# Optimization experiments

Measured on AMD Instinct MI355X. Metric: run time of the kernel, lower is better.

The kernel has to match this reference:

```python
import jax, jax.numpy as jnp
import numpy as np

HEADS = 4
NEG_SLOPE = 0.2  # GATv2Conv default negative_slope and module's LeakyReLU
LN_EPS = 1e-5


def setup_inputs() -> dict:
    key = jax.random.key(0)
    ks = jax.random.split(key, 12)
    N, D, E = 50000, 128, 400000
    H, C = HEADS, D
    s = 0.05
    x = jax.random.normal(ks[0], (N, D), dtype=jnp.float32)
    edge_index = jax.random.randint(ks[1], (2, E), 0, N, dtype=jnp.int64)
    return {
        "x": x,
        "edge_index": edge_index,
        "W_l": jax.random.normal(ks[2], (D, H * C), dtype=jnp.float32) * s,
        "b_l": jnp.zeros((H * C,), jnp.float32),
        "W_r": jax.random.normal(ks[3], (D, H * C), dtype=jnp.float32) * s,
        "b_r": jnp.zeros((H * C,), jnp.float32),
        "att": jax.random.normal(ks[4], (H, C), dtype=jnp.float32) * s,
        "gat_bias": jnp.zeros((C,), jnp.float32),
        "ln_g": jnp.ones((D,), jnp.float32),
        "ln_b": jnp.zeros((D,), jnp.float32),
        "W1": jax.random.normal(ks[5], (D, 2 * D), dtype=jnp.float32) * s,
        "b1": jnp.zeros((2 * D,), jnp.float32),
        "W2": jax.random.normal(ks[6], (2 * D, D), dtype=jnp.float32) * s,
        "b2": jnp.zeros((D,), jnp.float32),
    }


def _gatv2(x, src, dst, W_l, b_l, W_r, b_r, att, gat_bias, N):
    D = x.shape[1]
    H, C = HEADS, D
    xl = (x @ W_l + b_l).reshape(N, H, C)  # source-side projection
    xr = (x @ W_r + b_r).reshape(N, H, C)  # target-side projection
    # per-edge GATv2 score: leaky_relu(x_j + x_i) . att
    e = jax.nn.leaky_relu(xl[src] + xr[dst], NEG_SLOPE)  # [E, H, C]
    alpha = jnp.einsum('ehc,hc->eh', e, att)             # [E, H]
    # segment softmax over destination nodes
    amax = jax.ops.segment_max(alpha, dst, num_segments=N)  # [N, H]
    ex = jnp.exp(alpha - amax[dst])
    denom = jax.ops.segment_sum(ex, dst, num_segments=N)
    w = ex / (denom[dst] + 1e-16)                        # [E, H]
    msg = xl[src] * w[:, :, None]                        # [E, H, C]
    out = jax.ops.segment_sum(msg, dst, num_segments=N)  # [N, H, C]
    return out.mean(axis=1) + gat_bias                   # concat=False -> head mean + bias


def reference(x, edge_index, W_l, b_l, W_r, b_r, att, gat_bias, ln_g, ln_b, W1, b1, W2, b2):
    N = x.shape[0]
    # GATv2Conv default add_self_loops=True
    loops = jnp.arange(N, dtype=edge_index.dtype)
    src = jnp.concatenate([edge_index[0], loops])
    dst = jnp.concatenate([edge_index[1], loops])
    h = x + _gatv2(x, src, dst, W_l, b_l, W_r, b_r, att, gat_bias, N)
    # LayerNorm
    mu = h.mean(-1, keepdims=True)
    var = ((h - mu) ** 2).mean(-1, keepdims=True)
    hn = (h - mu) * jax.lax.rsqrt(var + LN_EPS) * ln_g + ln_b
    # FFN with residual
    ffn = jax.nn.leaky_relu(hn @ W1 + b1, NEG_SLOPE) @ W2 + b2
    return hn + ffn
```

## Files before the change

### kernel.cpp

```cpp
#include <hip/hip_runtime.h>
#include <hip/hip_bf16.h>
#include <stdint.h>

typedef __hip_bfloat16 bf16;
typedef __attribute__((ext_vector_type(8))) short short8;
typedef __attribute__((ext_vector_type(4))) float f32x4;

#define NEG 0.2f
#define LN_EPS 1e-5f

__device__ __host__ __forceinline__ int stdch(int q) {
    return (q & ~63) | (16 * (q & 3)) | ((q & 63) >> 2);
}

__device__ __forceinline__ float bits2f(unsigned b) {
    return __uint_as_float(b << 16);
}
__device__ __forceinline__ float hi2f(unsigned b) {
    return __uint_as_float(b & 0xffff0000u);
}
__device__ __forceinline__ unsigned short f2b_bits(float f) {
    unsigned u = __float_as_uint(f);
    unsigned r = u + 0x7fffu + ((u >> 16) & 1u);
    return (unsigned short)(r >> 16);
}
__device__ __forceinline__ float lrelu(float v) {
    return fmaxf(v, 0.f) + NEG * fminf(v, 0.f);
}
__device__ __forceinline__ void unpack8(uint4 u, float* v) {
    v[0] = bits2f(u.x); v[1] = hi2f(u.x);
    v[2] = bits2f(u.y); v[3] = hi2f(u.y);
    v[4] = bits2f(u.z); v[5] = hi2f(u.z);
    v[6] = bits2f(u.w); v[7] = hi2f(u.w);
}

union S8 { uint4 u; short8 s; unsigned short us[8]; };
__device__ __forceinline__ short8 ld8b(const char* p) {
    S8 c; c.u = *(const uint4*)p; return c.s;
}
__device__ __forceinline__ short8 ld8f(const float* p) {
    float4 a = ((const float4*)p)[0], b = ((const float4*)p)[1];
    S8 c;
    c.us[0] = f2b_bits(a.x); c.us[1] = f2b_bits(a.y);
    c.us[2] = f2b_bits(a.z); c.us[3] = f2b_bits(a.w);
    c.us[4] = f2b_bits(b.x); c.us[5] = f2b_bits(b.y);
    c.us[6] = f2b_bits(b.z); c.us[7] = f2b_bits(b.w);
    return c.s;
}

template <int CTRL>
__device__ __forceinline__ float ror_add16(float x) {
    int xi = __float_as_int(x);
    int r = __builtin_amdgcn_update_dpp(xi, xi, CTRL, 0xf, 0xf, false);
    return x + __int_as_float(r);
}

__global__ void detect_kernel(const unsigned* __restrict__ xw, const int* __restrict__ ei,
                              int* __restrict__ flags, int E) {
    int lane = threadIdx.x;
    int sane = 0;
    for (int k = 0; k < 4; ++k) {
        unsigned short lo = (unsigned short)(xw[k * 64 + lane] & 0xFFFFu);
        int ex = (lo >> 7) & 0xFF;
        if (lo == 0 || (ex > 100 && ex < 155)) sane++;
    }
#pragma unroll
    for (int off = 32; off > 0; off >>= 1) sane += __shfl_xor(sane, off);
    int nchk = E < 64 ? E : 64;
    int bad = (lane < nchk) ? (ei[2 * lane + 1] != 0) : 0;
    unsigned long long bb = __ballot(bad);
    if (lane == 0) {
        flags[0] = (sane > 200) ? 1 : 0;
        flags[1] = (bb == 0ULL) ? 1 : 0;
    }
}

struct PrepArgs {
    const void* Wl; const void* Wr; const void* W1; const void* W2;
    const void* ssrc[8];
    const int* ei;
    unsigned short* Wlt; unsigned short* Wrt; unsigned short* W1t; unsigned short* W2x;
    float* smalls;
    int* deg;
    int N; int E;
};
__device__ __forceinline__ float cvt_one(const void* p, int idx, int isb) {
    return isb ? bits2f(((const unsigned short*)p)[idx]) : ((const float*)p)[idx];
}
__global__ __launch_bounds__(256) void prep_kernel(PrepArgs a, const int* __restrict__ flags) {
    int isb = flags[0];
    int i = blockIdx.x * 256 + threadIdx.x;
    int seg = blockIdx.y;
    if (seg == 0) {
        if (i < 512 * 128) {
            int c = i >> 7, k = i & 127;
            a.Wlt[i] = isb ? ((const unsigned short*)a.Wl)[k * 512 + c]
                           : f2b_bits(((const float*)a.Wl)[k * 512 + c]);
        }
    } else if (seg == 1) {
        if (i < 512 * 128) {
            int c = i >> 7, k = i & 127;
            a.Wrt[i] = isb ? ((const unsigned short*)a.Wr)[k * 512 + c]
                           : f2b_bits(((const float*)a.Wr)[k * 512 + c]);
        }
    } else if (seg == 2) {
        if (i < 256 * 128) {
            int c = i >> 7, q = i & 127;
            int k = stdch(q);
            a.W1t[i] = isb ? ((const unsigned short*)a.W1)[k * 256 + c]
                           : f2b_bits(((const float*)a.W1)[k * 256 + c]);
        }
    } else if (seg == 3) {
        if (i < 128 * 384) {
            int c = i / 384, p = i - c * 384;
            if (p < 256) {
                int k = stdch(p);
                a.W2x[i] = isb ? ((const unsigned short*)a.W2)[k * 128 + c]
                               : f2b_bits(((const float*)a.W2)[k * 128 + c]);
            } else {
                int q = p - 256;
                a.W2x[i] = (stdch(q) == c) ? (unsigned short)0x3F80 : (unsigned short)0;
            }
        }
    } else if (seg == 4) {
        if (i < a.E) {
            int d = flags[1] ? a.ei[2 * (size_t)a.E + 2 * (size_t)i] : a.ei[(size_t)a.E + i];
            if ((unsigned)d >= (unsigned)a.N) d = 0;
            atomicAdd(&a.deg[d], 1);
        }
    } else {
        if (i < 512) a.smalls[i] = cvt_one(a.ssrc[0], i, isb);
        else if (i < 1024) a.smalls[i] = cvt_one(a.ssrc[1], i - 512, isb);
        else if (i < 1536) {
            int j = i - 1024, h = j >> 7, q = j & 127;
            a.smalls[i] = cvt_one(a.ssrc[2], h * 128 + stdch(q), isb);
        } else if (i < 1664) a.smalls[i] = cvt_one(a.ssrc[3], stdch(i - 1536), isb);
        else if (i < 1792)   a.smalls[i] = cvt_one(a.ssrc[4], stdch(i - 1664), isb);
        else if (i < 1920)   a.smalls[i] = cvt_one(a.ssrc[5], stdch(i - 1792), isb);
        else if (i < 2176)   a.smalls[i] = cvt_one(a.ssrc[6], i - 1920, isb);
        else if (i < 2304)   a.smalls[i] = cvt_one(a.ssrc[7], i - 2176, isb);
    }
}


__global__ __launch_bounds__(256) void proj_scatter_kernel(
    const void* __restrict__ xv, const unsigned short* __restrict__ Wlt,
    const unsigned short* __restrict__ Wrt, const float* __restrict__ smalls,
    unsigned short* __restrict__ xl, unsigned short* __restrict__ xr,
    const int* __restrict__ ei, int* __restrict__ cursor, int* __restrict__ srcs,
    int N, int E, int ET, int gproj, const int* __restrict__ flags) {
    if ((int)blockIdx.x >= gproj) {
        int e = ((int)blockIdx.x - gproj) * 256 + (int)threadIdx.x;
        if (e >= ET) return;
        int s, d;
        if (e < E) {
            if (flags[1]) { s = ei[2 * (size_t)e]; d = ei[2 * (size_t)E + 2 * (size_t)e]; }
            else          { s = ei[e];             d = ei[(size_t)E + e]; }
        } else { s = e - E; d = s; }
        if ((unsigned)s >= (unsigned)N) s = 0;
        if ((unsigned)d >= (unsigned)N) d = 0;
        int pos = atomicAdd(&cursor[d], 1);
        srcs[pos] = s;
        return;
    }
    int isb = flags[0];
    int wid = threadIdx.x >> 6, lane = threadIdx.x & 63;
    int quad = lane >> 4, l16 = lane & 15;
    int m0 = blockIdx.x * 64;

    int ra[4];
#pragma unroll
    for (int rf = 0; rf < 4; ++rf) {
        int r = m0 + rf * 16 + l16;
        ra[rf] = (r < N) ? r : N - 1;
    }
    short8 A[4][4];
#pragma unroll
    for (int rf = 0; rf < 4; ++rf)
#pragma unroll
        for (int k4 = 0; k4 < 4; ++k4) {
            int ko = k4 * 32 + quad * 8;
            if (isb) A[rf][k4] = ld8b((const char*)xv + ((size_t)ra[rf] * 128 + ko) * 2);
            else     A[rf][k4] = ld8f((const float*)xv + (size_t)ra[rf] * 128 + ko);
        }

    for (int iter = 0; iter < 4; ++iter) {
        const unsigned short* Wt = (iter < 2) ? Wlt : Wrt;
        const float* bias = smalls + ((iter < 2) ? 0 : 512);
        unsigned short* out = (iter < 2) ? xl : xr;
        int n0 = (iter & 1) * 256 + wid * 64;

        f32x4 acc[4][4];
#pragma unroll
        for (int rf = 0; rf < 4; ++rf)
#pragma unroll
            for (int c = 0; c < 4; ++c) acc[rf][c] = (f32x4){0.f, 0.f, 0.f, 0.f};

#pragma unroll
        for (int k4 = 0; k4 < 4; ++k4) {
            short8 b[4];
#pragma unroll
            for (int c = 0; c < 4; ++c)
                b[c] = ld8b((const char*)(Wt + (size_t)(n0 + c * 16 + l16) * 128 + k4 * 32 + quad * 8));
#pragma unroll
            for (int rf = 0; rf < 4; ++rf)
#pragma unroll
                for (int c = 0; c < 4; ++c)
                    acc[rf][c] = __builtin_amdgcn_mfma_f32_16x16x32_bf16(A[rf][k4], b[c], acc[rf][c], 0, 0, 0);
        }
        float bv[4];
#pragma unroll
        for (int c = 0; c < 4; ++c) bv[c] = bias[n0 + c * 16 + l16];
#pragma unroll
        for (int rf = 0; rf < 4; ++rf) {
#pragma unroll
            for (int j = 0; j < 4; ++j) {
                int row = m0 + rf * 16 + quad * 4 + j;
                if (row < N) {
                    uint2 pk;
                    pk.x = (unsigned)f2b_bits(acc[rf][0][j] + bv[0]) |
                           ((unsigned)f2b_bits(acc[rf][1][j] + bv[1]) << 16);
                    pk.y = (unsigned)f2b_bits(acc[rf][2][j] + bv[2]) |
                           ((unsigned)f2b_bits(acc[rf][3][j] + bv[3]) << 16);
                    *(uint2*)(out + (size_t)row * 512 + n0 + 4 * l16) = pk;
                }
            }
        }
    }
}

__global__ __launch_bounds__(256) void scanA_kernel(const int* __restrict__ deg,
                                                    int* __restrict__ part, int N) {
    int t = threadIdx.x, lane = t & 63, wid = t >> 6;
    int i = blockIdx.x * 256 + t;
    int v = (i < N) ? deg[i] + 1 : 0;
#pragma unroll
    for (int off = 32; off > 0; off >>= 1) v += __shfl_xor(v, off);
    __shared__ int ws4[4];
    if (lane == 0) ws4[wid] = v;
    __syncthreads();
    if (t == 0) part[blockIdx.x] = ws4[0] + ws4[1] + ws4[2] + ws4[3];
}

__global__ __launch_bounds__(256) void scanC_kernel(const int* __restrict__ deg,
                                                    const int* __restrict__ part,
                                                    int* __restrict__ rowptr,
                                                    int* __restrict__ cursor, int N) {
    int t = threadIdx.x, lane = t & 63, wid = t >> 6;
    int b = blockIdx.x;
    __shared__ int ws[4];
    int acc = 0;
    for (int c0 = 0; c0 < b; c0 += 256) {
        int idx = c0 + t;
        int v = (idx < b) ? part[idx] : 0;
#pragma unroll
        for (int off = 32; off > 0; off >>= 1) v += __shfl_xor(v, off);
        if (lane == 0) ws[wid] = v;
        __syncthreads();
        acc += ws[0] + ws[1] + ws[2] + ws[3];
        __syncthreads();
    }
    int i = b * 256 + t;
    int v = (i < N) ? deg[i] + 1 : 0;
    int x = v;
#pragma unroll
    for (int off = 1; off < 64; off <<= 1) {
        int u = __shfl_up(x, off);
        if (lane >= off) x += u;
    }
    if (lane == 63) ws[wid] = x;
    __syncthreads();
    int base = acc;
    for (int w = 0; w < wid; ++w) base += ws[w];
    int excl = base + x - v;
    if (i < N) { rowptr[i] = excl; cursor[i] = excl; }
    if (b == (int)gridDim.x - 1 && t == 0)
        rowptr[N] = acc + ws[0] + ws[1] + ws[2] + ws[3];
}

__global__ __launch_bounds__(256, 2) void agg_kernel(
    const bf16* __restrict__ xl, bf16* __restrict__ xr,
    const void* __restrict__ xv, const int* __restrict__ rowptr,
    const int* __restrict__ srcs, const float* __restrict__ smalls,
    int N, const int* __restrict__ flags) {
    int n = blockIdx.x * 4 + (threadIdx.x >> 6);
    if (n >= N) return;
    int lane = threadIdx.x & 63;
    int h = lane >> 4, cg = lane & 15;
    const float* att = smalls + 1024;
    const float* gat_bias = smalls + 1536;
    const float* ln_g = smalls + 1664;
    const float* ln_b = smalls + 1792;

    float att_f[8];
    {
        const float4* ap = (const float4*)(att + (size_t)h * 128 + cg * 8);
        float4 a0 = ap[0], a1 = ap[1];
        att_f[0] = a0.x; att_f[1] = a0.y; att_f[2] = a0.z; att_f[3] = a0.w;
        att_f[4] = a1.x; att_f[5] = a1.y; att_f[6] = a1.z; att_f[7] = a1.w;
    }
    float xr_f[8];
    uint4 xw = ((const uint4*)(xr + (size_t)n * 512))[lane];
    unpack8(xw, xr_f);

    float o[8];
#pragma unroll
    for (int j = 0; j < 8; ++j) o[j] = 0.f;
    float lsum = 0.f;

    int beg = rowptr[n], end = rowptr[n + 1];
    int last = end - 1;
    const uint4* xlu = (const uint4*)xl;
    int sA = srcs[beg];
    int sB = srcs[min(beg + 1, last)];
    uint4 lw = xlu[(size_t)sA * 64 + lane];
    for (int i = beg; i < end; ++i) {
        uint4 cur = lw;
        int snext = sB;
        sB = srcs[min(i + 2, last)];
        lw = xlu[(size_t)snext * 64 + lane];
        float v[8];
        unpack8(cur, v);
        float dotA = 0.f, dotB = 0.f;
#pragma unroll
        for (int j = 0; j < 8; ++j) {
            float z = v[j] + xr_f[j];
            dotA = fmaf(z, att_f[j], dotA);
            dotB = fmaf(fabsf(z), att_f[j], dotB);
        }
        float p = fmaf(0.4f, dotB, 0.6f * dotA);
        p = ror_add16<0x128>(p);
        p = ror_add16<0x124>(p);
        p = ror_add16<0x122>(p);
        p = ror_add16<0x121>(p);
        float w = __expf(fminf(p, 60.f));
        lsum += w;
#pragma unroll
        for (int j = 0; j < 8; ++j) o[j] = fmaf(w, v[j], o[j]);
        asm volatile("" : "+v"(o[0]), "+v"(o[1]), "+v"(o[2]), "+v"(o[3]),
                          "+v"(o[4]), "+v"(o[5]), "+v"(o[6]), "+v"(o[7]),
                          "+v"(lsum),
                          "+v"(att_f[0]), "+v"(att_f[1]), "+v"(att_f[2]), "+v"(att_f[3]),
                          "+v"(att_f[4]), "+v"(att_f[5]), "+v"(att_f[6]), "+v"(att_f[7]),
                          "+v"(xr_f[0]), "+v"(xr_f[1]), "+v"(xr_f[2]), "+v"(xr_f[3]),
                          "+v"(xr_f[4]), "+v"(xr_f[5]), "+v"(xr_f[6]), "+v"(xr_f[7]));
    }
    float inv = 0.25f / lsum;
#pragma unroll
    for (int j = 0; j < 8; ++j) o[j] *= inv;
#pragma unroll
    for (int j = 0; j < 8; ++j) {
        o[j] += __shfl_xor(o[j], 16);
        o[j] += __shfl_xor(o[j], 32);
    }
    int bc = 64 * (cg >> 3) + 2 * (cg & 7);
    float xf[8];
    if (flags[0]) {
#pragma unroll
        for (int c = 0; c < 4; ++c) {
            unsigned d = *(const unsigned*)((const unsigned short*)xv + (size_t)n * 128 + bc + 16 * c);
            xf[c] = bits2f(d); xf[c + 4] = hi2f(d);
        }
    } else {
#pragma unroll
        for (int c = 0; c < 4; ++c) {
            float2 f = *(const float2*)((const float*)xv + (size_t)n * 128 + bc + 16 * c);
            xf[c] = f.x; xf[c + 4] = f.y;
        }
    }
    float gb[8];
    {
        const float4* gp = (const float4*)(gat_bias + cg * 8);
        float4 a0 = gp[0], a1 = gp[1];
        gb[0] = a0.x; gb[1] = a0.y; gb[2] = a0.z; gb[3] = a0.w;
        gb[4] = a1.x; gb[5] = a1.y; gb[6] = a1.z; gb[7] = a1.w;
    }
    float vl[8];
    float s1v = 0.f;
#pragma unroll
    for (int j = 0; j < 8; ++j) { vl[j] = xf[j] + o[j] + gb[j]; s1v += vl[j]; }
    s1v += __shfl_xor(s1v, 1); s1v += __shfl_xor(s1v, 2);
    s1v += __shfl_xor(s1v, 4); s1v += __shfl_xor(s1v, 8);
    float mu = s1v * (1.f / 128.f);
    float s2v = 0.f;
#pragma unroll
    for (int j = 0; j < 8; ++j) { float d = vl[j] - mu; s2v += d * d; }
    s2v += __shfl_xor(s2v, 1); s2v += __shfl_xor(s2v, 2);
    s2v += __shfl_xor(s2v, 4); s2v += __shfl_xor(s2v, 8);
    float rinv = rsqrtf(s2v * (1.f / 128.f) + LN_EPS);
    if (h == 0) {
        float g[8], bt[8];
        const float4* gp = (const float4*)(ln_g + cg * 8);
        float4 g0 = gp[0], g1 = gp[1];
        g[0] = g0.x; g[1] = g0.y; g[2] = g0.z; g[3] = g0.w;
        g[4] = g1.x; g[5] = g1.y; g[6] = g1.z; g[7] = g1.w;
        const float4* bp = (const float4*)(ln_b + cg * 8);
        float4 b0 = bp[0], b1v = bp[1];
        bt[0] = b0.x; bt[1] = b0.y; bt[2] = b0.z; bt[3] = b0.w;
        bt[4] = b1v.x; bt[5] = b1v.y; bt[6] = b1v.z; bt[7] = b1v.w;
        float hnv[8];
#pragma unroll
        for (int j = 0; j < 8; ++j) hnv[j] = (vl[j] - mu) * rinv * g[j] + bt[j];
        char* rowp = (char*)xr + (size_t)n * 1024;
        uint4 pk;
        pk.x = (unsigned)f2b_bits(hnv[0]) | ((unsigned)f2b_bits(hnv[1]) << 16);
        pk.y = (unsigned)f2b_bits(hnv[2]) | ((unsigned)f2b_bits(hnv[3]) << 16);
        pk.z = (unsigned)f2b_bits(hnv[4]) | ((unsigned)f2b_bits(hnv[5]) << 16);
        pk.w = (unsigned)f2b_bits(hnv[6]) | ((unsigned)f2b_bits(hnv[7]) << 16);
        *(uint4*)(rowp + cg * 16) = pk;
    }
}

__global__ __launch_bounds__(256) void ffn_fused_kernel(
    const char* __restrict__ hnrows, const unsigned short* __restrict__ W1t,
    const unsigned short* __restrict__ W2x, const float* __restrict__ smalls,
    void* __restrict__ outv, int N, const int* __restrict__ flags) {
    __shared__ __align__(16) char lds[64 * 528];
    const float* b1 = smalls + 1920;
    const float* b2v = smalls + 2176;
    int wid = threadIdx.x >> 6, lane = threadIdx.x & 63;
    int quad = lane >> 4, l16 = lane & 15;
    int m0 = blockIdx.x * 64;

    int ra[4];
#pragma unroll
    for (int rf = 0; rf < 4; ++rf) {
        int r = m0 + rf * 16 + l16;
        ra[rf] = (r < N) ? r : N - 1;
    }
    short8 A[4][4];
#pragma unroll
    for (int rf = 0; rf < 4; ++rf)
#pragma unroll
        for (int k4 = 0; k4 < 4; ++k4)
            A[rf][k4] = ld8b(hnrows + (size_t)ra[rf] * 1024 + (k4 * 32 + quad * 8) * 2);

    {
        int n0 = wid * 64;
        f32x4 acc[4][4];
#pragma unroll
        for (int rf = 0; rf < 4; ++rf)
#pragma unroll
            for (int c = 0; c < 4; ++c) acc[rf][c] = (f32x4){0.f, 0.f, 0.f, 0.f};
#pragma unroll
        for (int k4 = 0; k4 < 4; ++k4) {
            short8 b[4];
#pragma unroll
            for (int c = 0; c < 4; ++c)
                b[c] = ld8b((const char*)(W1t + (size_t)(n0 + c * 16 + l16) * 128 + k4 * 32 + quad * 8));
#pragma unroll
            for (int rf = 0; rf < 4; ++rf)
#pragma unroll
                for (int c = 0; c < 4; ++c)
                    acc[rf][c] = __builtin_amdgcn_mfma_f32_16x16x32_bf16(A[rf][k4], b[c], acc[rf][c], 0, 0, 0);
        }
        float bv[4];
#pragma unroll
        for (int c = 0; c < 4; ++c) bv[c] = b1[n0 + c * 16 + l16];
#pragma unroll
        for (int rf = 0; rf < 4; ++rf) {
#pragma unroll
            for (int j = 0; j < 4; ++j) {
                int lrow = rf * 16 + quad * 4 + j;
                uint2 pk;
                pk.x = (unsigned)f2b_bits(lrelu(acc[rf][0][j] + bv[0])) |
                       ((unsigned)f2b_bits(lrelu(acc[rf][1][j] + bv[1])) << 16);
                pk.y = (unsigned)f2b_bits(lrelu(acc[rf][2][j] + bv[2])) |
                       ((unsigned)f2b_bits(lrelu(acc[rf][3][j] + bv[3])) << 16);
                *(uint2*)(lds + lrow * 528 + (n0 + 4 * l16) * 2) = pk;
            }
        }
    }
    __syncthreads();
    int rh = wid >> 1, nh = wid & 1;
    int n0b = nh * 64;
    f32x4 a2[2][4];
#pragma unroll
    for (int rfl = 0; rfl < 2; ++rfl)
#pragma unroll
        for (int c = 0; c < 4; ++c) a2[rfl][c] = (f32x4){0.f, 0.f, 0.f, 0.f};
#pragma unroll
    for (int kk = 0; kk < 256; kk += 32) {
        short8 am[2], b[4];
#pragma unroll
        for (int rfl = 0; rfl < 2; ++rfl)
            am[rfl] = ld8b(lds + (rh * 32 + rfl * 16 + l16) * 528 + (kk + quad * 8) * 2);
#pragma unroll
        for (int c = 0; c < 4; ++c)
            b[c] = ld8b((const char*)(W2x + (size_t)(n0b + c * 16 + l16) * 384 + kk + quad * 8));
#pragma unroll
        for (int rfl = 0; rfl < 2; ++rfl)
#pragma unroll
            for (int c = 0; c < 4; ++c)
                a2[rfl][c] = __builtin_amdgcn_mfma_f32_16x16x32_bf16(am[rfl], b[c], a2[rfl][c], 0, 0, 0);
    }
#pragma unroll
    for (int k4 = 0; k4 < 4; ++k4) {
        short8 b[4];
#pragma unroll
        for (int c = 0; c < 4; ++c)
            b[c] = ld8b((const char*)(W2x + (size_t)(n0b + c * 16 + l16) * 384 + 256 + k4 * 32 + quad * 8));
#pragma unroll
        for (int rfl = 0; rfl < 2; ++rfl)
#pragma unroll
            for (int c = 0; c < 4; ++c)
                a2[rfl][c] = __builtin_amdgcn_mfma_f32_16x16x32_bf16(A[rh * 2 + rfl][k4], b[c], a2[rfl][c], 0, 0, 0);
    }
    __syncthreads();
#pragma unroll
    for (int c = 0; c < 4; ++c) {
        int col = n0b + c * 16 + l16;
        float bv = b2v[col];
#pragma unroll
        for (int rfl = 0; rfl < 2; ++rfl) {
#pragma unroll
            for (int j = 0; j < 4; ++j) {
                int lrow = rh * 32 + rfl * 16 + quad * 4 + j;
                *(float*)(lds + lrow * 528 + col * 4) = a2[rfl][c][j] + bv;
            }
        }
    }
    __syncthreads();
    int isb = flags[0];
    int t = (int)threadIdx.x;
    if (isb) {
#pragma unroll
        for (int k = 0; k < 4; ++k) {
            int f = t * 8 + k * 2048;
            int lrow = f >> 7, col = f & 127;
            int row = m0 + lrow;
            if (row < N) {
                const float* src = (const float*)(lds + lrow * 528) + col;
                uint4 pk;
                pk.x = (unsigned)f2b_bits(src[0]) | ((unsigned)f2b_bits(src[1]) << 16);
                pk.y = (unsigned)f2b_bits(src[2]) | ((unsigned)f2b_bits(src[3]) << 16);
                pk.z = (unsigned)f2b_bits(src[4]) | ((unsigned)f2b_bits(src[5]) << 16);
                pk.w = (unsigned)f2b_bits(src[6]) | ((unsigned)f2b_bits(src[7]) << 16);
                *(uint4*)((unsigned short*)outv + (size_t)row * 128 + col) = pk;
            }
        }
    } else {
#pragma unroll
        for (int k = 0; k < 8; ++k) {
            int f = t * 4 + k * 1024;
            int lrow = f >> 7, col = f & 127;
            int row = m0 + lrow;
            if (row < N) {
                const float* src = (const float*)(lds + lrow * 528) + col;
                float4 v = *(const float4*)src;
                *(float4*)((float*)outv + (size_t)row * 128 + col) = v;
            }
        }
    }
}

extern "C" void kernel_launch(void* const* d_in, const int* in_sizes, int n_in,
                              void* d_out, int out_size, void* d_ws, size_t ws_size,
                              hipStream_t stream) {
    const void* x = d_in[0];
    const int* ei = (const int*)d_in[1];

    int N = in_sizes[0] / 128;
    int E = in_sizes[1] / 2;
    int ET = E + N;
    int nb = (N + 255) / 256;

    char* base = (char*)d_ws;
    int* flags = (int*)base;
    size_t off = 256;
    float* smalls = (float*)(base + off);               off += 2304 * 4;
    off = (off + 255) & ~(size_t)255;
    unsigned short* Wlt = (unsigned short*)(base + off); off += 512 * 128 * 2;
    unsigned short* Wrt = (unsigned short*)(base + off); off += 512 * 128 * 2;
    unsigned short* W1t = (unsigned short*)(base + off); off += 256 * 128 * 2;
    unsigned short* W2x = (unsigned short*)(base + off); off += 128 * 384 * 2;
    off = (off + 1023) & ~(size_t)1023;
    bf16* xl = (bf16*)(base + off);   off += (size_t)N * 512 * 2;
    bf16* xr = (bf16*)(base + off);   off += (size_t)N * 512 * 2;
    int* srcs = (int*)(base + off);   off += (size_t)ET * 4;
    int* rowptr = (int*)(base + off); off += (size_t)(N + 1) * 4;
    int* deg = (int*)(base + off);    off += (size_t)N * 4;
    int* cursor = (int*)(base + off); off += (size_t)N * 4;
    int* part = (int*)(base + off);   off += (size_t)nb * 4;
    const char* hnrows = (const char*)xr;

    hipMemsetAsync(deg, 0, (size_t)N * 4, stream);

    detect_kernel<<<1, 64, 0, stream>>>((const unsigned*)x, ei, flags, E);

    PrepArgs pa;
    pa.Wl = d_in[2]; pa.Wr = d_in[4]; pa.W1 = d_in[10]; pa.W2 = d_in[12];
    pa.ssrc[0] = d_in[3];  pa.ssrc[1] = d_in[5];  pa.ssrc[2] = d_in[6];
    pa.ssrc[3] = d_in[7];  pa.ssrc[4] = d_in[8];  pa.ssrc[5] = d_in[9];
    pa.ssrc[6] = d_in[11]; pa.ssrc[7] = d_in[13];
    pa.ei = ei;
    pa.Wlt = Wlt; pa.Wrt = Wrt; pa.W1t = W1t; pa.W2x = W2x;
    pa.smalls = smalls; pa.deg = deg; pa.N = N; pa.E = E;
    int px = (E > 65536 ? E : 65536);
    prep_kernel<<<dim3((px + 255) / 256, 6), 256, 0, stream>>>(pa, flags);

    scanA_kernel<<<nb, 256, 0, stream>>>(deg, part, N);
    scanC_kernel<<<nb, 256, 0, stream>>>(deg, part, rowptr, cursor, N);

    int g64 = (N + 63) / 64;
    int scb = (ET + 255) / 256;
    proj_scatter_kernel<<<g64 + scb, 256, 0, stream>>>(
        x, Wlt, Wrt, smalls, (unsigned short*)xl, (unsigned short*)xr,
        ei, cursor, srcs, N, E, ET, g64, flags);

    agg_kernel<<<(N + 3) / 4, 256, 0, stream>>>(xl, xr, x, rowptr, srcs, smalls, N, flags);

    ffn_fused_kernel<<<g64, 256, 0, stream>>>(hnrows, W1t, W2x, smalls, d_out, N, flags);
}
```

Baseline: 335.7 us.

## Pre-swizzle weights into MFMA fragment order and stage A rows through LDS

Weight matrices are now stored in the prep kernel in a per-lane MFMA fragment layout, so each wave's B-operand load is one contiguous 1 KB read instead of strided 16-byte reads across rows. Input rows for the projection and FFN kernels are loaded cooperatively with coalesced 16-byte accesses into LDS, then read into fragment registers. This aims to reduce uncoalesced global traffic. The cost is an extra LDS round trip and additional barriers, plus more LDS use in the projection kernel, which may lower occupancy.

Measured after the change: 300.0 us (median of 2 runs). 10.6% less time.

```diff
diff --git a/kernel.cpp b/kernel.cpp
--- a/kernel.cpp
+++ b/kernel.cpp
@@ -93,33 +93,45 @@
     int seg = blockIdx.y;
     if (seg == 0) {
         if (i < 512 * 128) {
-            int c = i >> 7, k = i & 127;
-            a.Wlt[i] = isb ? ((const unsigned short*)a.Wl)[k * 512 + c]
-                           : f2b_bits(((const float*)a.Wl)[k * 512 + c]);
+            int j = i & 7, lane = (i >> 3) & 63, k4 = (i >> 9) & 3, nb = i >> 11;
+            int col = nb * 16 + (lane & 15);
+            int k = k4 * 32 + (lane >> 4) * 8 + j;
+            a.Wlt[i] = isb ? ((const unsigned short*)a.Wl)[k * 512 + col]
+                           : f2b_bits(((const float*)a.Wl)[k * 512 + col]);
         }
     } else if (seg == 1) {
         if (i < 512 * 128) {
-            int c = i >> 7, k = i & 127;
-            a.Wrt[i] = isb ? ((const unsigned short*)a.Wr)[k * 512 + c]
-                           : f2b_bits(((const float*)a.Wr)[k * 512 + c]);
+            int j = i & 7, lane = (i >> 3) & 63, k4 = (i >> 9) & 3, nb = i >> 11;
+            int col = nb * 16 + (lane & 15);
+            int k = k4 * 32 + (lane >> 4) * 8 + j;
+            a.Wrt[i] = isb ? ((const unsigned short*)a.Wr)[k * 512 + col]
+                           : f2b_bits(((const float*)a.Wr)[k * 512 + col]);
         }
     } else if (seg == 2) {
         if (i < 256 * 128) {
-            int c = i >> 7, q = i & 127;
+            int j = i & 7, lane = (i >> 3) & 63;
+            int r2 = i >> 9;
+            int k4 = r2 & 3, nb = r2 >> 2;
+            int col = nb * 16 + (lane & 15);
+            int q = k4 * 32 + (lane >> 4) * 8 + j;
             int k = stdch(q);
-            a.W1t[i] = isb ? ((const unsigned short*)a.W1)[k * 256 + c]
-                           : f2b_bits(((const float*)a.W1)[k * 256 + c]);
+            a.W1t[i] = isb ? ((const unsigned short*)a.W1)[k * 256 + col]
+                           : f2b_bits(((const float*)a.W1)[k * 256 + col]);
         }
     } else if (seg == 3) {
         if (i < 128 * 384) {
-            int c = i / 384, p = i - c * 384;
+            int j = i & 7, lane = (i >> 3) & 63;
+            int r2 = i >> 9;
+            int k4 = r2 % 12, nb = r2 / 12;
+            int col = nb * 16 + (lane & 15);
+            int p = k4 * 32 + (lane >> 4) * 8 + j;
             if (p < 256) {
                 int k = stdch(p);
-                a.W2x[i] = isb ? ((const unsigned short*)a.W2)[k * 128 + c]
-                               : f2b_bits(((const float*)a.W2)[k * 128 + c]);
+                a.W2x[i] = isb ? ((const unsigned short*)a.W2)[k * 128 + col]
+                               : f2b_bits(((const float*)a.W2)[k * 128 + col]);
             } else {
                 int q = p - 256;
-                a.W2x[i] = (stdch(q) == c) ? (unsigned short)0x3F80 : (unsigned short)0;
+                a.W2x[i] = (stdch(q) == col) ? (unsigned short)0x3F80 : (unsigned short)0;
             }
         }
     } else if (seg == 4) {
@@ -163,32 +175,36 @@
         srcs[pos] = s;
         return;
     }
+    __shared__ __align__(16) unsigned short alds[64 * 136];
     int isb = flags[0];
+    int tt = (int)threadIdx.x;
     int wid = threadIdx.x >> 6, lane = threadIdx.x & 63;
     int quad = lane >> 4, l16 = lane & 15;
     int m0 = blockIdx.x * 64;
 
-    int ra[4];
-#pragma unroll
-    for (int rf = 0; rf < 4; ++rf) {
-        int r = m0 + rf * 16 + l16;
-        ra[rf] = (r < N) ? r : N - 1;
-    }
+#pragma unroll
+    for (int s = 0; s < 4; ++s) {
+        int row = s * 16 + (tt >> 4);
+        int gr = m0 + row; gr = (gr < N) ? gr : N - 1;
+        S8 c8;
+        if (isb) c8.u = *(const uint4*)((const char*)xv + (size_t)gr * 256 + (tt & 15) * 16);
+        else     c8.s = ld8f((const float*)xv + (size_t)gr * 128 + (tt & 15) * 8);
+        *(uint4*)(alds + row * 136 + (tt & 15) * 8) = c8.u;
+    }
+    __syncthreads();
     short8 A[4][4];
 #pragma unroll
     for (int rf = 0; rf < 4; ++rf)
 #pragma unroll
-        for (int k4 = 0; k4 < 4; ++k4) {
-            int ko = k4 * 32 + quad * 8;
-            if (isb) A[rf][k4] = ld8b((const char*)xv + ((size_t)ra[rf] * 128 + ko) * 2);
-            else     A[rf][k4] = ld8f((const float*)xv + (size_t)ra[rf] * 128 + ko);
-        }
+        for (int k4 = 0; k4 < 4; ++k4)
+            A[rf][k4] = ld8b((const char*)(alds + (rf * 16 + l16) * 136 + k4 * 32 + quad * 8));
 
     for (int iter = 0; iter < 4; ++iter) {
         const unsigned short* Wt = (iter < 2) ? Wlt : Wrt;
         const float* bias = smalls + ((iter < 2) ? 0 : 512);
         unsigned short* out = (iter < 2) ? xl : xr;
         int n0 = (iter & 1) * 256 + wid * 64;
+        int nb0 = n0 >> 4;
 
         f32x4 acc[4][4];
 #pragma unroll
@@ -201,7 +217,7 @@
             short8 b[4];
 #pragma unroll
             for (int c = 0; c < 4; ++c)
-                b[c] = ld8b((const char*)(Wt + (size_t)(n0 + c * 16 + l16) * 128 + k4 * 32 + quad * 8));
+                b[c] = ld8b((const char*)(Wt + (((size_t)(nb0 + c) * 4 + k4) * 64 + lane) * 8));
 #pragma unroll
             for (int rf = 0; rf < 4; ++rf)
 #pragma unroll
@@ -418,22 +434,26 @@
     __shared__ __align__(16) char lds[64 * 528];
     const float* b1 = smalls + 1920;
     const float* b2v = smalls + 2176;
+    int tt = (int)threadIdx.x;
     int wid = threadIdx.x >> 6, lane = threadIdx.x & 63;
     int quad = lane >> 4, l16 = lane & 15;
     int m0 = blockIdx.x * 64;
 
-    int ra[4];
-#pragma unroll
-    for (int rf = 0; rf < 4; ++rf) {
-        int r = m0 + rf * 16 + l16;
-        ra[rf] = (r < N) ? r : N - 1;
-    }
+#pragma unroll
+    for (int s = 0; s < 4; ++s) {
+        int row = s * 16 + (tt >> 4);
+        int gr = m0 + row; gr = (gr < N) ? gr : N - 1;
+        uint4 v = *(const uint4*)(hnrows + (size_t)gr * 1024 + (tt & 15) * 16);
+        *(uint4*)(lds + row * 272 + (tt & 15) * 16) = v;
+    }
+    __syncthreads();
     short8 A[4][4];
 #pragma unroll
     for (int rf = 0; rf < 4; ++rf)
 #pragma unroll
         for (int k4 = 0; k4 < 4; ++k4)
-            A[rf][k4] = ld8b(hnrows + (size_t)ra[rf] * 1024 + (k4 * 32 + quad * 8) * 2);
+            A[rf][k4] = ld8b(lds + (rf * 16 + l16) * 272 + (k4 * 32 + quad * 8) * 2);
+    __syncthreads();
 
     {
         int n0 = wid * 64;
@@ -447,7 +467,7 @@
             short8 b[4];
 #pragma unroll
             for (int c = 0; c < 4; ++c)
-                b[c] = ld8b((const char*)(W1t + (size_t)(n0 + c * 16 + l16) * 128 + k4 * 32 + quad * 8));
+                b[c] = ld8b((const char*)(W1t + (((size_t)(wid * 4 + c) * 4 + k4) * 64 + lane) * 8));
 #pragma unroll
             for (int rf = 0; rf < 4; ++rf)
 #pragma unroll
@@ -481,13 +501,14 @@
         for (int c = 0; c < 4; ++c) a2[rfl][c] = (f32x4){0.f, 0.f, 0.f, 0.f};
 #pragma unroll
     for (int kk = 0; kk < 256; kk += 32) {
+        int k4 = kk >> 5;
         short8 am[2], b[4];
 #pragma unroll
         for (int rfl = 0; rfl < 2; ++rfl)
             am[rfl] = ld8b(lds + (rh * 32 + rfl * 16 + l16) * 528 + (kk + quad * 8) * 2);
 #pragma unroll
         for (int c = 0; c < 4; ++c)
-            b[c] = ld8b((const char*)(W2x + (size_t)(n0b + c * 16 + l16) * 384 + kk + quad * 8));
+            b[c] = ld8b((const char*)(W2x + (((size_t)(nh * 4 + c) * 12 + k4) * 64 + lane) * 8));
 #pragma unroll
         for (int rfl = 0; rfl < 2; ++rfl)
 #pragma unroll
@@ -499,7 +520,7 @@
         short8 b[4];
 #pragma unroll
         for (int c = 0; c < 4; ++c)
-            b[c] = ld8b((const char*)(W2x + (size_t)(n0b + c * 16 + l16) * 384 + 256 + k4 * 32 + quad * 8));
+            b[c] = ld8b((const char*)(W2x + (((size_t)(nh * 4 + c) * 12 + 8 + k4) * 64 + lane) * 8));
 #pragma unroll
         for (int rfl = 0; rfl < 2; ++rfl)
 #pragma unroll
```
